# Optimization experiments

Hardware: AMD Instinct MI355X
Metric: run time of the kernel (lower is better)

## Reference

```python
import jax, jax.numpy as jnp
import numpy as np

B, H, W, C = 2, 96, 192, 768
NH, HD = 12, 64
W0, W1 = 8, 8          # window size
S0, S1 = 4, 4          # shift size
N = W0 * W1
NW = (H // W0) * (W // W1)
HID = 3072             # mlp_ratio 4 * dim
SCALE = HD ** -0.5


def _ln(x, g, b):
    m = x.mean(-1, keepdims=True)
    v = ((x - m) ** 2).mean(-1, keepdims=True)
    return (x - m) * jax.lax.rsqrt(v + 1e-5) * g + b


def _partition(x):  # (B,H,W,C) -> (B*NW, W0, W1, C)
    Bb = x.shape[0]
    x = x.reshape(Bb, H // W0, W0, W // W1, W1, -1).transpose(0, 1, 3, 2, 4, 5)
    return x.reshape(-1, W0, W1, x.shape[-1])


def _reverse(w):  # (B*NW, W0, W1, C) -> (B,H,W,C)
    Cc = w.shape[-1]
    x = w.reshape(B, H // W0, W // W1, W0, W1, Cc).transpose(0, 1, 3, 2, 4, 5)
    return x.reshape(B, H, W, Cc)


def _rope2(x):  # axial 2D RoPE on (nB, W0, W1, HD): first half rotates over h, second over w
    dh = HD // 2

    def cs(L, d):
        inv = 1.0 / (10000.0 ** (jnp.arange(0, d, 2, dtype=jnp.float32) / d))
        ang = jnp.arange(L, dtype=jnp.float32)[:, None] * inv
        return jnp.cos(ang), jnp.sin(ang)

    def rot(xa, cos, sin):
        x1, x2 = xa[..., 0::2], xa[..., 1::2]
        return jnp.stack([x1 * cos - x2 * sin, x1 * sin + x2 * cos], -1).reshape(xa.shape)

    ch, sh = cs(W0, dh)
    cw, sw = cs(W1, dh)
    xh = rot(x[..., :dh], ch[:, None, :], sh[:, None, :])
    xw = rot(x[..., dh:], cw[None, :, :], sw[None, :, :])
    return jnp.concatenate([xh, xw], -1)


def _make_mask():
    # faithful port of BasicLayer.create_mask (2D path)
    img = np.zeros((H, W), np.float32)
    cnt = 0
    for hs in (slice(0, -W0), slice(-W0, -S0), slice(-S0, None)):
        for wsl in (slice(0, -W1), slice(-W1, 0), slice(0, None)):
            img[hs, wsl] = cnt
            cnt += 1
    mw = img.reshape(H // W0, W0, W // W1, W1).transpose(0, 2, 1, 3).reshape(NW, N)
    am = mw[:, None, :] - mw[:, :, None]
    return jnp.asarray(np.where(am != 0, -100.0, 0.0).astype(np.float32))


def setup_inputs():
    key = jax.random.key(0)
    ks = jax.random.split(key, 6)
    s = lambda k, shape, fan: jax.random.normal(k, shape, jnp.float32) * (fan ** -0.5)
    return dict(
        x=jax.random.normal(ks[0], (B, H * W, C), jnp.float32),
        mask=_make_mask(),
        w_qkv=s(ks[1], (3 * C, C), C), b_qkv=jnp.zeros((3 * C,), jnp.float32),
        w_proj=s(ks[2], (C, C), C), b_proj=jnp.zeros((C,), jnp.float32),
        g1=jnp.ones((C,), jnp.float32), b1=jnp.zeros((C,), jnp.float32),
        g2=jnp.ones((C,), jnp.float32), b2=jnp.zeros((C,), jnp.float32),
        w_fc1=s(ks[3], (HID, C), C), b_fc1=jnp.zeros((HID,), jnp.float32),
        w_fc2=s(ks[4], (C, HID), HID), b_fc2=jnp.zeros((C,), jnp.float32),
    )


def reference(x, mask, w_qkv, b_qkv, w_proj, b_proj, g1, b1, g2, b2,
              w_fc1, b_fc1, w_fc2, b_fc2):
    shortcut = x
    xi = x.reshape(B, H, W, C)
    xi = jnp.roll(xi, (-S0, -S1), axis=(1, 2))
    xw = _partition(xi).reshape(-1, N, C)  # (B*NW, N, C)
    B_ = xw.shape[0]
    qkv = (xw @ w_qkv.T + b_qkv).reshape(B_, N, 3, NH, HD).transpose(2, 0, 3, 1, 4)
    q, k, v = qkv[0], qkv[1], qkv[2]  # (B_, NH, N, HD)
    q = _rope2(q.reshape(-1, W0, W1, HD)).reshape(B_, NH, N, HD)
    k = _rope2(k.reshape(-1, W0, W1, HD)).reshape(B_, NH, N, HD)
    attn = jnp.einsum('bhnd,bhmd->bhnm', q * SCALE, k)
    attn = attn.reshape(B, NW, NH, N, N) + mask[None, :, None]
    attn = jax.nn.softmax(attn.reshape(B_, NH, N, N), axis=-1)
    out = jnp.einsum('bhnm,bhmd->bnhd', attn, v).reshape(B_, N, C)
    out = out @ w_proj.T + b_proj
    xr = _reverse(out.reshape(-1, W0, W1, C))
    xr = jnp.roll(xr, (S0, S1), axis=(1, 2)).reshape(B, H * W, C)
    x1 = _ln(shortcut + xr, g1, b1)          # post-norm residual, as in source
    h = jax.nn.relu(x1 @ w_fc1.T + b_fc1) @ w_fc2.T + b_fc2
    return _ln(x1 + h, g2, b2)
```

## Files before the change

### kernel.cpp

```cpp
#include <hip/hip_runtime.h>
#include <math.h>
#include <stddef.h>

#define NTOK   36864
#define CDIM   768
#define HIDDIM 3072
#define QKVDIM 2304

typedef unsigned short u16;
typedef unsigned int   u32;
typedef __attribute__((ext_vector_type(8))) short short8;
typedef __attribute__((ext_vector_type(4))) float f32x4;

__device__ __forceinline__ float bf2f(u16 h) { return __uint_as_float(((u32)h) << 16); }
__device__ __forceinline__ u16 f2bf(float f) {
  u32 u = __float_as_uint(f);
  u32 r = u + 0x7fffu + ((u >> 16) & 1u);
  return (u16)(r >> 16);
}

__device__ __forceinline__ int win_row_to_src(int r) {
  int n = r & 63;
  int wflat = r >> 6;
  int b = wflat / 288;
  int wi = wflat - b * 288;
  int wh = wi / 24;
  int ww = wi - wh * 24;
  int i0 = n >> 3, i1 = n & 7;
  int hh = wh * 8 + i0 + 4; if (hh >= 96)  hh -= 96;
  int wp = ww * 8 + i1 + 4; if (wp >= 192) wp -= 192;
  return b * 18432 + hh * 192 + wp;
}

__device__ __forceinline__ void load_lds16(const u16* g, u16* l) {
  __builtin_amdgcn_global_load_lds((const __attribute__((address_space(1))) void*)g,
                                   (__attribute__((address_space(3))) void*)l, 16, 0, 0);
}

template<int OUTBF, int RELU, int RES>
__launch_bounds__(512, 2)
__global__ void gemm256(const u16* __restrict__ A, const u16* __restrict__ Wt,
                        const float* __restrict__ bias, const u16* __restrict__ res,
                        void* __restrict__ Cout, int M, int N, int K,
                        int gridx, int nwg)
{
  const int orig = blockIdx.x;
  const int xcd  = orig & 7;
  const int q    = nwg >> 3, r8 = nwg & 7;
  const int wgid = (xcd < r8 ? xcd * (q + 1) : r8 * (q + 1) + (xcd - r8) * q) + (orig >> 3);
  const int bn   = (wgid % gridx) * 256;
  const int bm   = (wgid / gridx) * 256;

  __shared__ __align__(16) u16 lds[2][2][256 * 64];

  const int t    = threadIdx.x;
  const int wv   = t >> 6, lane = t & 63;
  const int wm   = wv >> 2, wn = wv & 3;
  const int lr   = lane & 15, lg = lane >> 4;
  const int sr   = t >> 3;
  const int ss   = t & 7;

  const u16* Abase = A  + (size_t)bm * K;
  const u16* Bbase = Wt + (size_t)bn * K;

  const int nt = K >> 6;

  auto stage = [&](int kt, int b) {
    const int k0 = kt << 6;
#pragma unroll
    for (int j = 0; j < 4; j++) {
      int row  = j * 64 + sr;
      int slot = ss ^ (row & 7);
      load_lds16(Abase + (size_t)row * K + k0 + slot * 8, &lds[b][0][j * 4096 + t * 8]);
    }
#pragma unroll
    for (int j = 0; j < 4; j++) {
      int row  = j * 64 + sr;
      int slot = ss ^ (row & 7);
      load_lds16(Bbase + (size_t)row * K + k0 + slot * 8, &lds[b][1][j * 4096 + t * 8]);
    }
  };

  f32x4 acc[8][4] = {};

  stage(0, 0);
  stage(1, 1);

  for (int tt = 0; tt < nt; tt++) {
    const int cur = tt & 1;
    if (tt + 1 < nt) asm volatile("s_waitcnt vmcnt(8)" ::: "memory");
    else             asm volatile("s_waitcnt vmcnt(0)" ::: "memory");
    __builtin_amdgcn_s_barrier();

    const u16* Ab = &lds[cur][0][0];
    const u16* Bb = &lds[cur][1][0];

    short8 bfr[4][2], afr[4][2];
#pragma unroll
    for (int nf = 0; nf < 4; nf++)
#pragma unroll
      for (int ks = 0; ks < 2; ks++) {
        int row = wn * 64 + nf * 16 + lr;
        bfr[nf][ks] = *(const short8*)(Bb + row * 64 + (((ks * 4 + lg) ^ (row & 7)) << 3));
      }
#pragma unroll
    for (int mf = 0; mf < 4; mf++)
#pragma unroll
      for (int ks = 0; ks < 2; ks++) {
        int row = wm * 128 + mf * 16 + lr;
        afr[mf][ks] = *(const short8*)(Ab + row * 64 + (((ks * 4 + lg) ^ (row & 7)) << 3));
      }
    asm volatile("s_waitcnt lgkmcnt(0)" ::: "memory");
    __builtin_amdgcn_sched_barrier(0);
    __builtin_amdgcn_s_setprio(1);
#pragma unroll
    for (int ks = 0; ks < 2; ks++)
#pragma unroll
      for (int mf = 0; mf < 4; mf++)
#pragma unroll
        for (int nf = 0; nf < 4; nf++)
          acc[mf][nf] = __builtin_amdgcn_mfma_f32_16x16x32_bf16(afr[mf][ks], bfr[nf][ks], acc[mf][nf], 0, 0, 0);
    __builtin_amdgcn_s_setprio(0);

    short8 afr2[4][2];
#pragma unroll
    for (int mf = 0; mf < 4; mf++)
#pragma unroll
      for (int ks = 0; ks < 2; ks++) {
        int row = wm * 128 + (mf + 4) * 16 + lr;
        afr2[mf][ks] = *(const short8*)(Ab + row * 64 + (((ks * 4 + lg) ^ (row & 7)) << 3));
      }
    asm volatile("s_waitcnt lgkmcnt(0)" ::: "memory");
    __builtin_amdgcn_sched_barrier(0);
    __builtin_amdgcn_s_barrier();

    if (tt + 2 < nt) stage(tt + 2, cur);

    __builtin_amdgcn_s_setprio(1);
#pragma unroll
    for (int ks = 0; ks < 2; ks++)
#pragma unroll
      for (int mf = 0; mf < 4; mf++)
#pragma unroll
        for (int nf = 0; nf < 4; nf++)
          acc[mf + 4][nf] = __builtin_amdgcn_mfma_f32_16x16x32_bf16(afr2[mf][ks], bfr[nf][ks], acc[mf + 4][nf], 0, 0, 0);
    __builtin_amdgcn_s_setprio(0);
  }

#pragma unroll
  for (int nf = 0; nf < 4; nf++) {
    int col = bn + wn * 64 + nf * 16 + lr;
    float bcol = bias[col];
#pragma unroll
    for (int mf = 0; mf < 8; mf++) {
#pragma unroll
      for (int j = 0; j < 4; j++) {
        int row = bm + wm * 128 + mf * 16 + lg * 4 + j;
        float v = acc[mf][nf][j] + bcol;
        if (RELU) v = fmaxf(v, 0.f);
        if (RES)  v += bf2f(res[(size_t)row * N + col]);
        if (OUTBF) ((u16*)Cout)[(size_t)row * N + col] = f2bf(v);
        else       ((float*)Cout)[(size_t)row * N + col] = v;
      }
    }
  }
}

__launch_bounds__(256)
__global__ void gather_x_bf16(const float* __restrict__ x, u16* __restrict__ xg)
{
  const int r = blockIdx.x, t = threadIdx.x;
  const float* src = x + (size_t)win_row_to_src(r) * CDIM;
  u16* dst = xg + (size_t)r * CDIM;
#pragma unroll
  for (int e = 0; e < 3; e++) dst[t + 256 * e] = f2bf(src[t + 256 * e]);
}

__launch_bounds__(256)
__global__ void conv_bf16(const float* __restrict__ in, u16* __restrict__ out, int n)
{
  int i = blockIdx.x * 256 + threadIdx.x;
  if (i < n) out[i] = f2bf(in[i]);
}

__launch_bounds__(256)
__global__ void attn_mfma(const u16* __restrict__ qkv, const float* __restrict__ mask,
                          u16* __restrict__ out, int bw0)
{
  __shared__ u16 vt[4][4096];
  __shared__ u16 pbuf[4][4096];
  __shared__ float ropetab[512];

  const int t = threadIdx.x;
  {
    int p = t >> 3, pos = t & 7;
    float inv = __expf(-(float)(p & 15) * 0.5756462732485115f);
    float sv, cv;
    sincosf((float)pos * inv, &sv, &cv);
    ropetab[t * 2]     = cv;
    ropetab[t * 2 + 1] = sv;
  }
  __syncthreads();

  const int wv = t >> 6, lane = t & 63;
  const int lr = lane & 15, lg = lane >> 4;
  const int gp   = blockIdx.x * 4 + wv;
  const int head = gp % 12;
  const int lw   = gp / 12;
  const int bwg  = bw0 + lw;
  const int widx = bwg % 288;
  const u16* base = qkv + (size_t)lw * 64 * QKVDIM + head * 64;

  {
    const u16* vrow = base + 1536 + (size_t)lane * QKVDIM;
    u16* vb = vt[wv];
#pragma unroll
    for (int s = 0; s < 8; s++) {
      short8 v = *(const short8*)(vrow + s * 8);
#pragma unroll
      for (int j = 0; j < 8; j++) {
        int d = s * 8 + j;
        vb[d * 64 + ((((lane >> 3) ^ (d & 7)) << 3) | (lane & 7))] = (u16)v[j];
      }
    }
  }

  short8 aq[4][2], ak[4][2];
#pragma unroll
  for (int f = 0; f < 4; f++) {
#pragma unroll
    for (int ks = 0; ks < 2; ks++) {
      int n = f * 16 + lr;
      short8 qv = *(const short8*)(base + (size_t)n * QKVDIM + ks * 32 + lg * 8);
      short8 kv = *(const short8*)(base + (size_t)n * QKVDIM + 768 + ks * 32 + lg * 8);
      short8 qo, ko;
#pragma unroll
      for (int jj = 0; jj < 4; jj++) {
        int p   = ks * 16 + lg * 4 + jj;
        int pos = (p < 16) ? (n >> 3) : (n & 7);
        float cv = ropetab[(p * 8 + pos) * 2];
        float sv = ropetab[(p * 8 + pos) * 2 + 1];
        float q1 = bf2f((u16)qv[2 * jj]), q2 = bf2f((u16)qv[2 * jj + 1]);
        float k1 = bf2f((u16)kv[2 * jj]), k2 = bf2f((u16)kv[2 * jj + 1]);
        qo[2 * jj]     = (short)f2bf((q1 * cv - q2 * sv) * 0.125f);
        qo[2 * jj + 1] = (short)f2bf((q1 * sv + q2 * cv) * 0.125f);
        ko[2 * jj]     = (short)f2bf(k1 * cv - k2 * sv);
        ko[2 * jj + 1] = (short)f2bf(k1 * sv + k2 * cv);
      }
      aq[f][ks] = qo; ak[f][ks] = ko;
    }
  }

  f32x4 sf[4][4] = {};
#pragma unroll
  for (int ks = 0; ks < 2; ks++)
#pragma unroll
    for (int fn = 0; fn < 4; fn++)
#pragma unroll
      for (int fm = 0; fm < 4; fm++)
        sf[fn][fm] = __builtin_amdgcn_mfma_f32_16x16x32_bf16(aq[fn][ks], ak[fm][ks], sf[fn][fm], 0, 0, 0);

  const float* mrow = mask + (size_t)widx * 4096;
#pragma unroll
  for (int fn = 0; fn < 4; fn++)
#pragma unroll
    for (int fm = 0; fm < 4; fm++)
#pragma unroll
      for (int j = 0; j < 4; j++)
        sf[fn][fm][j] += mrow[(fn * 16 + lg * 4 + j) * 64 + fm * 16 + lr];

#pragma unroll
  for (int fn = 0; fn < 4; fn++) {
#pragma unroll
    for (int j = 0; j < 4; j++) {
      float m0 = fmaxf(fmaxf(sf[fn][0][j], sf[fn][1][j]),
                       fmaxf(sf[fn][2][j], sf[fn][3][j]));
      m0 = fmaxf(m0, __shfl_xor(m0, 1));
      m0 = fmaxf(m0, __shfl_xor(m0, 2));
      m0 = fmaxf(m0, __shfl_xor(m0, 4));
      m0 = fmaxf(m0, __shfl_xor(m0, 8));
      float s0 = 0.f;
#pragma unroll
      for (int fm = 0; fm < 4; fm++) {
        float e = __expf(sf[fn][fm][j] - m0);
        sf[fn][fm][j] = e;
        s0 += e;
      }
      s0 += __shfl_xor(s0, 1);
      s0 += __shfl_xor(s0, 2);
      s0 += __shfl_xor(s0, 4);
      s0 += __shfl_xor(s0, 8);
      float r = 1.f / s0;
#pragma unroll
      for (int fm = 0; fm < 4; fm++) sf[fn][fm][j] *= r;
    }
  }

  u16* pb = pbuf[wv];
#pragma unroll
  for (int fn = 0; fn < 4; fn++)
#pragma unroll
    for (int fm = 0; fm < 4; fm++)
#pragma unroll
      for (int j = 0; j < 4; j++) {
        int n = fn * 16 + lg * 4 + j, m = fm * 16 + lr;
        pb[n * 64 + ((((m >> 3) ^ (n & 7)) << 3) | (m & 7))] = f2bf(sf[fn][fm][j]);
      }
  asm volatile("s_waitcnt lgkmcnt(0)" ::: "memory");
  __builtin_amdgcn_sched_barrier(0);

  short8 ap[4][2], bvf[4][2];
#pragma unroll
  for (int f = 0; f < 4; f++)
#pragma unroll
    for (int ks = 0; ks < 2; ks++) {
      int rn = f * 16 + lr;
      ap[f][ks]  = *(const short8*)(pb     + rn * 64 + (((ks * 4 + lg) ^ (rn & 7)) << 3));
      bvf[f][ks] = *(const short8*)(vt[wv] + rn * 64 + (((ks * 4 + lg) ^ (rn & 7)) << 3));
    }
  f32x4 o[4][4] = {};
#pragma unroll
  for (int ks = 0; ks < 2; ks++)
#pragma unroll
    for (int fn = 0; fn < 4; fn++)
#pragma unroll
      for (int fd = 0; fd < 4; fd++)
        o[fn][fd] = __builtin_amdgcn_mfma_f32_16x16x32_bf16(ap[fn][ks], bvf[fd][ks], o[fn][fd], 0, 0, 0);

  u16* ob = out + ((size_t)bwg * 64) * CDIM + head * 64;
#pragma unroll
  for (int fn = 0; fn < 4; fn++)
#pragma unroll
    for (int fd = 0; fd < 4; fd++)
#pragma unroll
      for (int j = 0; j < 4; j++) {
        int n = fn * 16 + lg * 4 + j, d = fd * 16 + lr;
        ob[(size_t)n * CDIM + d] = f2bf(o[fn][fd][j]);
      }
}

__launch_bounds__(256)
__global__ void ln1_kernel(const float* __restrict__ xin, const u16* __restrict__ add,
                           const float* __restrict__ g, const float* __restrict__ bb,
                           u16* __restrict__ out)
{
  const int tok = blockIdx.x;
  int b = tok / 18432;
  int hw = tok - b * 18432;
  int h = hw / 192, w = hw - h * 192;
  int h2 = h - 4; if (h2 < 0) h2 += 96;
  int w2 = w - 4; if (w2 < 0) w2 += 192;
  int r = ((b * 12 + (h2 >> 3)) * 24 + (w2 >> 3)) * 64 + (h2 & 7) * 8 + (w2 & 7);
  const float* a0 = xin + (size_t)tok * CDIM;
  const u16*   a1 = add + (size_t)r * CDIM;

  const int t = threadIdx.x;
  float v[3];
  float s1 = 0.f, s2 = 0.f;
#pragma unroll
  for (int e = 0; e < 3; e++) {
    float x = a0[t + 256 * e] + bf2f(a1[t + 256 * e]);
    v[e] = x; s1 += x; s2 += x * x;
  }
  __shared__ float r1[256], r2[256];
  r1[t] = s1; r2[t] = s2;
  __syncthreads();
  for (int o = 128; o > 0; o >>= 1) {
    if (t < o) { r1[t] += r1[t + o]; r2[t] += r2[t + o]; }
    __syncthreads();
  }
  float mean = r1[0] * (1.f / 768.f);
  float var  = r2[0] * (1.f / 768.f) - mean * mean;
  float rs   = rsqrtf(var + 1e-5f);
#pragma unroll
  for (int e = 0; e < 3; e++) {
    int c = t + 256 * e;
    out[(size_t)tok * CDIM + c] = f2bf((v[e] - mean) * rs * g[c] + bb[c]);
  }
}

__launch_bounds__(256)
__global__ void ln2_kernel(const u16* __restrict__ xin, const float* __restrict__ g,
                           const float* __restrict__ bb, float* __restrict__ out)
{
  const int tok = blockIdx.x;
  const u16* a0 = xin + (size_t)tok * CDIM;
  const int t = threadIdx.x;
  float v[3];
  float s1 = 0.f, s2 = 0.f;
#pragma unroll
  for (int e = 0; e < 3; e++) {
    float x = bf2f(a0[t + 256 * e]);
    v[e] = x; s1 += x; s2 += x * x;
  }
  __shared__ float r1[256], r2[256];
  r1[t] = s1; r2[t] = s2;
  __syncthreads();
  for (int o = 128; o > 0; o >>= 1) {
    if (t < o) { r1[t] += r1[t + o]; r2[t] += r2[t + o]; }
    __syncthreads();
  }
  float mean = r1[0] * (1.f / 768.f);
  float var  = r2[0] * (1.f / 768.f) - mean * mean;
  float rs   = rsqrtf(var + 1e-5f);
#pragma unroll
  for (int e = 0; e < 3; e++) {
    int c = t + 256 * e;
    out[(size_t)tok * CDIM + c] = (v[e] - mean) * rs * g[c] + bb[c];
  }
}

static inline void launch_gemm(const u16* A, const u16* Wt, const float* bias,
                               const u16* res, void* C, int M, int N, int K,
                               int outbf, int relu, int resf, hipStream_t s)
{
  int gridx = N / 256, nwg = gridx * (M / 256);
  if (outbf) {
    if (relu)      gemm256<1,1,0><<<nwg, 512, 0, s>>>(A, Wt, bias, res, C, M, N, K, gridx, nwg);
    else if (resf) gemm256<1,0,1><<<nwg, 512, 0, s>>>(A, Wt, bias, res, C, M, N, K, gridx, nwg);
    else           gemm256<1,0,0><<<nwg, 512, 0, s>>>(A, Wt, bias, res, C, M, N, K, gridx, nwg);
  } else {
    gemm256<0,0,0><<<nwg, 512, 0, s>>>(A, Wt, bias, res, C, M, N, K, gridx, nwg);
  }
}

extern "C" void kernel_launch(void* const* d_in, const int* in_sizes, int n_in,
                              void* d_out, int out_size, void* d_ws, size_t ws_size,
                              hipStream_t stream)
{
  const float* x      = (const float*)d_in[0];
  const float* mask   = (const float*)d_in[1];
  const float* w_qkv  = (const float*)d_in[2];
  const float* b_qkv  = (const float*)d_in[3];
  const float* w_proj = (const float*)d_in[4];
  const float* b_proj = (const float*)d_in[5];
  const float* g1     = (const float*)d_in[6];
  const float* b1     = (const float*)d_in[7];
  const float* g2     = (const float*)d_in[8];
  const float* b2     = (const float*)d_in[9];
  const float* w_fc1  = (const float*)d_in[10];
  const float* b_fc1  = (const float*)d_in[11];
  const float* w_fc2  = (const float*)d_in[12];
  const float* b_fc2  = (const float*)d_in[13];
  float* out = (float*)d_out;

  char* base = (char*)d_ws;
  u16* R1 = (u16*)base;
  u16* R2 = (u16*)(base + 56623104);
  u16* AO = R2 + 28311552;
  u16* R3 = (u16*)(base + 56623104 + 113246208);
  u16* wqkvb  = (u16*)(base + 56623104 + 113246208 + 56623104);
  u16* wprojb = wqkvb  + 1769472;
  u16* wfc1b  = wprojb + 589824;
  u16* wfc2b  = wfc1b  + 2359296;

  conv_bf16<<<(1769472 + 255) / 256, 256, 0, stream>>>(w_qkv,  wqkvb,  1769472);
  conv_bf16<<<( 589824 + 255) / 256, 256, 0, stream>>>(w_proj, wprojb,  589824);
  conv_bf16<<<(2359296 + 255) / 256, 256, 0, stream>>>(w_fc1,  wfc1b,  2359296);
  conv_bf16<<<(2359296 + 255) / 256, 256, 0, stream>>>(w_fc2,  wfc2b,  2359296);
  gather_x_bf16<<<NTOK, 256, 0, stream>>>(x, R1);

  for (int c = 0; c < 3; c++) {
    launch_gemm(R1 + (size_t)c * 12288 * CDIM, wqkvb, b_qkv, nullptr, R2,
                12288, QKVDIM, CDIM, 1, 0, 0, stream);
    attn_mfma<<<576, 256, 0, stream>>>(R2, mask, AO, c * 192);
  }

  launch_gemm(AO, wprojb, b_proj, nullptr, R3, NTOK, CDIM, CDIM, 1, 0, 0, stream);

  ln1_kernel<<<NTOK, 256, 0, stream>>>(x, R3, g1, b1, R1);

  for (int c = 0; c < 2; c++) {
    const u16* x1c = R1 + (size_t)c * 18432 * CDIM;
    launch_gemm(x1c, wfc1b, b_fc1, nullptr, R2, 18432, HIDDIM, CDIM, 1, 1, 0, stream);
    launch_gemm(R2, wfc2b, b_fc2, x1c, R3 + (size_t)c * 18432 * CDIM,
                18432, CDIM, HIDDIM, 1, 0, 1, stream);
  }

  ln2_kernel<<<NTOK, 256, 0, stream>>>(R3, g2, b2, out);
}
```

Baseline: 953.8 us.

## Unchunk QKV/attention, vectorize LN and gather, remap GEMM tile order

Replaces the three-chunk QKV GEMM plus attention loop with a single full-size QKV GEMM and one attention launch over all windows, which needs a larger workspace layout. The gather, LN1 and LN2 kernels now give one row per wavefront, use vector loads and stores, and reduce with wave shuffles instead of an LDS tree with block barriers. The GEMM workgroup-to-tile mapping splits the N dimension into two halves to change L2 reuse patterns. The aim is fewer launches, less synchronisation and better memory efficiency, at the cost of a larger workspace footprint.

```diff
diff --git a/kernel.cpp b/kernel.cpp
--- a/kernel.cpp
+++ b/kernel.cpp
@@ -10,6 +10,7 @@
 typedef unsigned short u16;
 typedef unsigned int   u32;
 typedef __attribute__((ext_vector_type(8))) short short8;
+typedef __attribute__((ext_vector_type(4))) short short4v;
 typedef __attribute__((ext_vector_type(4))) float f32x4;
 
 __device__ __forceinline__ float bf2f(u16 h) { return __uint_as_float(((u32)h) << 16); }
@@ -48,8 +49,17 @@
   const int xcd  = orig & 7;
   const int q    = nwg >> 3, r8 = nwg & 7;
   const int wgid = (xcd < r8 ? xcd * (q + 1) : r8 * (q + 1) + (xcd - r8) * q) + (orig >> 3);
-  const int bn   = (wgid % gridx) * 256;
-  const int bm   = (wgid / gridx) * 256;
+  int bn, bm;
+  if (((gridx | nwg) & 1) == 0) {
+    const int halfn = nwg >> 1, hc = gridx >> 1;
+    const int half  = (wgid >= halfn) ? 1 : 0;
+    const int w2    = wgid - half * halfn;
+    bn = (w2 % hc + half * hc) * 256;
+    bm = (w2 / hc) * 256;
+  } else {
+    bn = (wgid % gridx) * 256;
+    bm = (wgid / gridx) * 256;
+  }
 
   __shared__ __align__(16) u16 lds[2][2][256 * 64];
 
@@ -169,11 +179,18 @@
 __launch_bounds__(256)
 __global__ void gather_x_bf16(const float* __restrict__ x, u16* __restrict__ xg)
 {
-  const int r = blockIdx.x, t = threadIdx.x;
-  const float* src = x + (size_t)win_row_to_src(r) * CDIM;
-  u16* dst = xg + (size_t)r * CDIM;
-#pragma unroll
-  for (int e = 0; e < 3; e++) dst[t + 256 * e] = f2bf(src[t + 256 * e]);
+  const int t = threadIdx.x, wv = t >> 6, lane = t & 63;
+  const int r = blockIdx.x * 4 + wv;
+  const float4* src = (const float4*)(x + (size_t)win_row_to_src(r) * CDIM);
+  short4v* dst = (short4v*)(xg + (size_t)r * CDIM);
+#pragma unroll
+  for (int e = 0; e < 3; e++) {
+    float4 f = src[e * 64 + lane];
+    short4v o;
+    o[0] = (short)f2bf(f.x); o[1] = (short)f2bf(f.y);
+    o[2] = (short)f2bf(f.z); o[3] = (short)f2bf(f.w);
+    dst[e * 64 + lane] = o;
+  }
 }
 
 __launch_bounds__(256)
@@ -185,7 +202,7 @@
 
 __launch_bounds__(256)
 __global__ void attn_mfma(const u16* __restrict__ qkv, const float* __restrict__ mask,
-                          u16* __restrict__ out, int bw0)
+                          u16* __restrict__ out)
 {
   __shared__ u16 vt[4][4096];
   __shared__ u16 pbuf[4][4096];
@@ -207,8 +224,7 @@
   const int gp   = blockIdx.x * 4 + wv;
   const int head = gp % 12;
   const int lw   = gp / 12;
-  const int bwg  = bw0 + lw;
-  const int widx = bwg % 288;
+  const int widx = lw % 288;
   const u16* base = qkv + (size_t)lw * 64 * QKVDIM + head * 64;
 
   {
@@ -327,7 +343,7 @@
       for (int fd = 0; fd < 4; fd++)
         o[fn][fd] = __builtin_amdgcn_mfma_f32_16x16x32_bf16(ap[fn][ks], bvf[fd][ks], o[fn][fd], 0, 0, 0);
 
-  u16* ob = out + ((size_t)bwg * 64) * CDIM + head * 64;
+  u16* ob = out + ((size_t)lw * 64) * CDIM + head * 64;
 #pragma unroll
   for (int fn = 0; fn < 4; fn++)
 #pragma unroll
@@ -344,38 +360,49 @@
                            const float* __restrict__ g, const float* __restrict__ bb,
                            u16* __restrict__ out)
 {
-  const int tok = blockIdx.x;
+  const int t = threadIdx.x, wv = t >> 6, lane = t & 63;
+  const int tok = blockIdx.x * 4 + wv;
   int b = tok / 18432;
   int hw = tok - b * 18432;
   int h = hw / 192, w = hw - h * 192;
   int h2 = h - 4; if (h2 < 0) h2 += 96;
   int w2 = w - 4; if (w2 < 0) w2 += 192;
   int r = ((b * 12 + (h2 >> 3)) * 24 + (w2 >> 3)) * 64 + (h2 & 7) * 8 + (w2 & 7);
-  const float* a0 = xin + (size_t)tok * CDIM;
-  const u16*   a1 = add + (size_t)r * CDIM;
-
-  const int t = threadIdx.x;
-  float v[3];
+  const float4*  a0 = (const float4*)(xin + (size_t)tok * CDIM);
+  const short4v* a1 = (const short4v*)(add + (size_t)r * CDIM);
+
+  float v[12];
   float s1 = 0.f, s2 = 0.f;
 #pragma unroll
   for (int e = 0; e < 3; e++) {
-    float x = a0[t + 256 * e] + bf2f(a1[t + 256 * e]);
-    v[e] = x; s1 += x; s2 += x * x;
-  }
-  __shared__ float r1[256], r2[256];
-  r1[t] = s1; r2[t] = s2;
-  __syncthreads();
-  for (int o = 128; o > 0; o >>= 1) {
-    if (t < o) { r1[t] += r1[t + o]; r2[t] += r2[t + o]; }
-    __syncthreads();
-  }
-  float mean = r1[0] * (1.f / 768.f);
-  float var  = r2[0] * (1.f / 768.f) - mean * mean;
+    float4  f = a0[e * 64 + lane];
+    short4v a = a1[e * 64 + lane];
+    float x0 = f.x + bf2f((u16)a[0]);
+    float x1 = f.y + bf2f((u16)a[1]);
+    float x2 = f.z + bf2f((u16)a[2]);
+    float x3 = f.w + bf2f((u16)a[3]);
+    v[e*4+0] = x0; v[e*4+1] = x1; v[e*4+2] = x2; v[e*4+3] = x3;
+    s1 += x0 + x1 + x2 + x3;
+    s2 += x0*x0 + x1*x1 + x2*x2 + x3*x3;
+  }
+#pragma unroll
+  for (int m = 1; m < 64; m <<= 1) {
+    s1 += __shfl_xor(s1, m);
+    s2 += __shfl_xor(s2, m);
+  }
+  float mean = s1 * (1.f / 768.f);
+  float var  = s2 * (1.f / 768.f) - mean * mean;
   float rs   = rsqrtf(var + 1e-5f);
+  short4v* dst = (short4v*)(out + (size_t)tok * CDIM);
 #pragma unroll
   for (int e = 0; e < 3; e++) {
-    int c = t + 256 * e;
-    out[(size_t)tok * CDIM + c] = f2bf((v[e] - mean) * rs * g[c] + bb[c]);
+    short4v o;
+#pragma unroll
+    for (int j = 0; j < 4; j++) {
+      int c = (e * 64 + lane) * 4 + j;
+      o[j] = (short)f2bf((v[e*4+j] - mean) * rs * g[c] + bb[c]);
+    }
+    dst[e * 64 + lane] = o;
   }
 }
 
@@ -383,30 +410,39 @@
 __global__ void ln2_kernel(const u16* __restrict__ xin, const float* __restrict__ g,
                            const float* __restrict__ bb, float* __restrict__ out)
 {
-  const int tok = blockIdx.x;
-  const u16* a0 = xin + (size_t)tok * CDIM;
-  const int t = threadIdx.x;
-  float v[3];
+  const int t = threadIdx.x, wv = t >> 6, lane = t & 63;
+  const int tok = blockIdx.x * 4 + wv;
+  const short4v* a0 = (const short4v*)(xin + (size_t)tok * CDIM);
+
+  float v[12];
   float s1 = 0.f, s2 = 0.f;
 #pragma unroll
   for (int e = 0; e < 3; e++) {
-    float x = bf2f(a0[t + 256 * e]);
-    v[e] = x; s1 += x; s2 += x * x;
-  }
-  __shared__ float r1[256], r2[256];
-  r1[t] = s1; r2[t] = s2;
-  __syncthreads();
-  for (int o = 128; o > 0; o >>= 1) {
-    if (t < o) { r1[t] += r1[t + o]; r2[t] += r2[t + o]; }
-    __syncthreads();
-  }
-  float mean = r1[0] * (1.f / 768.f);
-  float var  = r2[0] * (1.f / 768.f) - mean * mean;
+    short4v a = a0[e * 64 + lane];
+#pragma unroll
+    for (int j = 0; j < 4; j++) {
+      float x = bf2f((u16)a[j]);
+      v[e*4+j] = x; s1 += x; s2 += x * x;
+    }
+  }
+#pragma unroll
+  for (int m = 1; m < 64; m <<= 1) {
+    s1 += __shfl_xor(s1, m);
+    s2 += __shfl_xor(s2, m);
+  }
+  float mean = s1 * (1.f / 768.f);
+  float var  = s2 * (1.f / 768.f) - mean * mean;
   float rs   = rsqrtf(var + 1e-5f);
+  float4* dst = (float4*)(out + (size_t)tok * CDIM);
 #pragma unroll
   for (int e = 0; e < 3; e++) {
-    int c = t + 256 * e;
-    out[(size_t)tok * CDIM + c] = (v[e] - mean) * rs * g[c] + bb[c];
+    float4 o;
+    int c = (e * 64 + lane) * 4;
+    o.x = (v[e*4+0] - mean) * rs * g[c+0] + bb[c+0];
+    o.y = (v[e*4+1] - mean) * rs * g[c+1] + bb[c+1];
+    o.z = (v[e*4+2] - mean) * rs * g[c+2] + bb[c+2];
+    o.w = (v[e*4+3] - mean) * rs * g[c+3] + bb[c+3];
+    dst[e * 64 + lane] = o;
   }
 }
 
@@ -445,11 +481,12 @@
   float* out = (float*)d_out;
 
   char* base = (char*)d_ws;
-  u16* R1 = (u16*)base;
-  u16* R2 = (u16*)(base + 56623104);
-  u16* AO = R2 + 28311552;
-  u16* R3 = (u16*)(base + 56623104 + 113246208);
-  u16* wqkvb  = (u16*)(base + 56623104 + 113246208 + 56623104);
+  u16* P1  = (u16*)base;
+  u16* QKV = (u16*)(base + 56623104);
+  u16* Hb  = QKV;
+  u16* Yb  = (u16*)(base + 56623104 + 113246208);
+  u16* P3  = (u16*)(base + 56623104 + 169869312);
+  u16* wqkvb  = (u16*)(base + 56623104 + 169869312 + 56623104);
   u16* wprojb = wqkvb  + 1769472;
   u16* wfc1b  = wprojb + 589824;
   u16* wfc2b  = wfc1b  + 2359296;
@@ -458,24 +495,21 @@
   conv_bf16<<<( 589824 + 255) / 256, 256, 0, stream>>>(w_proj, wprojb,  589824);
   conv_bf16<<<(2359296 + 255) / 256, 256, 0, stream>>>(w_fc1,  wfc1b,  2359296);
   conv_bf16<<<(2359296 + 255) / 256, 256, 0, stream>>>(w_fc2,  wfc2b,  2359296);
-  gather_x_bf16<<<NTOK, 256, 0, stream>>>(x, R1);
-
-  for (int c = 0; c < 3; c++) {
-    launch_gemm(R1 + (size_t)c * 12288 * CDIM, wqkvb, b_qkv, nullptr, R2,
-                12288, QKVDIM, CDIM, 1, 0, 0, stream);
-    attn_mfma<<<576, 256, 0, stream>>>(R2, mask, AO, c * 192);
-  }
-
-  launch_gemm(AO, wprojb, b_proj, nullptr, R3, NTOK, CDIM, CDIM, 1, 0, 0, stream);
-
-  ln1_kernel<<<NTOK, 256, 0, stream>>>(x, R3, g1, b1, R1);
+  gather_x_bf16<<<NTOK / 4, 256, 0, stream>>>(x, P1);
+
+  launch_gemm(P1, wqkvb, b_qkv, nullptr, QKV, NTOK, QKVDIM, CDIM, 1, 0, 0, stream);
+  attn_mfma<<<576 * 12 / 4, 256, 0, stream>>>(QKV, mask, P1);
+
+  launch_gemm(P1, wprojb, b_proj, nullptr, P3, NTOK, CDIM, CDIM, 1, 0, 0, stream);
+
+  ln1_kernel<<<NTOK / 4, 256, 0, stream>>>(x, P3, g1, b1, P1);
 
   for (int c = 0; c < 2; c++) {
-    const u16* x1c = R1 + (size_t)c * 18432 * CDIM;
-    launch_gemm(x1c, wfc1b, b_fc1, nullptr, R2, 18432, HIDDIM, CDIM, 1, 1, 0, stream);
-    launch_gemm(R2, wfc2b, b_fc2, x1c, R3 + (size_t)c * 18432 * CDIM,
+    const u16* x1c = P1 + (size_t)c * 18432 * CDIM;
+    launch_gemm(x1c, wfc1b, b_fc1, nullptr, Hb, 18432, HIDDIM, CDIM, 1, 1, 0, stream);
+    launch_gemm(Hb, wfc2b, b_fc2, x1c, Yb + (size_t)c * 18432 * CDIM,
                 18432, CDIM, HIDDIM, 1, 0, 1, stream);
   }
 
-  ln2_kernel<<<NTOK, 256, 0, stream>>>(R3, g2, b2, out);
-}
+  ln2_kernel<<<NTOK / 4, 256, 0, stream>>>(Yb, g2, b2, out);
+}
```

After: 913.1 us. -4.3%, faster.
